# Kernel optimization log

Measured on AMD Instinct MI355X. Metric: run time of the kernel, lower is better.

## Reference

```python
import jax, jax.numpy as jnp
import numpy as np

# dims
B, L, H, W, C = 1, 5, 100, 176, 256   # batch, agents, BEV height, BEV width, channels
HEADS, DHEAD, T = 8, 32, 3            # heads, per-head dim, num agent types
D = HEADS * DHEAD                     # == C here (to_qkv inner dim)
SCALE = DHEAD ** -0.5


def setup_inputs() -> dict:
    key = jax.random.key(0)
    ks = jax.random.split(key, 14)
    x = jax.random.normal(ks[0], (B, L, H, W, C), jnp.float32)
    mask = jnp.ones((B, H, W, 1, L), jnp.int32)
    types = jax.random.randint(ks[1], (B, L), 0, T)
    # prior_encoding: [B, L, 1, 1, 3] = (velocity, dt, type); only type (channel 2) is used
    prior_encoding = jnp.zeros((B, L, 1, 1, 3), jnp.float32).at[..., 2].set(
        types[:, :, None, None].astype(jnp.float32))
    s = C ** -0.5
    Wq = jax.random.normal(ks[2], (T, C, D), jnp.float32) * s
    bq = jax.random.normal(ks[3], (T, D), jnp.float32) * 0.01
    Wk = jax.random.normal(ks[4], (T, C, D), jnp.float32) * s
    bk = jax.random.normal(ks[5], (T, D), jnp.float32) * 0.01
    Wv = jax.random.normal(ks[6], (T, C, D), jnp.float32) * s
    bv = jax.random.normal(ks[7], (T, D), jnp.float32) * 0.01
    Wa = jax.random.normal(ks[8], (T, D, C), jnp.float32) * (D ** -0.5)
    ba = jax.random.normal(ks[9], (T, C), jnp.float32) * 0.01
    rel_att = jax.random.normal(ks[10], (T * T, HEADS, DHEAD, DHEAD), jnp.float32) * (DHEAD ** -0.5)
    rel_msg = jax.random.normal(ks[11], (T * T, HEADS, DHEAD, DHEAD), jnp.float32) * (DHEAD ** -0.5)
    return dict(x=x, mask=mask, prior_encoding=prior_encoding,
                Wq=Wq, bq=bq, Wk=Wk, bk=bk, Wv=Wv, bv=bv, Wa=Wa, ba=ba,
                rel_att=rel_att, rel_msg=rel_msg)


def _split_heads(t):
    # [B,H,W,L,D] -> [B,m,H,W,L,p]
    return jnp.transpose(t.reshape(B, H, W, L, HEADS, DHEAD), (0, 4, 1, 2, 3, 5))


def reference(x, mask, prior_encoding, Wq, bq, Wk, bk, Wv, bv, Wa, ba, rel_att, rel_msg):
    types = prior_encoding[:, :, 0, 0, 2].astype(jnp.int32)      # [B,L]
    xp = jnp.transpose(x, (0, 2, 3, 1, 4))                        # [B,H,W,L,C]

    def proj(Wt, bt):
        # per-agent-type linear: gather weights per agent, then batched matmul
        return jnp.einsum('bhwlc,blcd->bhwld', xp, Wt[types]) + bt[types][:, None, None]

    q = _split_heads(proj(Wq, bq))                                # [B,m,H,W,L,p]
    k = _split_heads(proj(Wk, bk))
    v = _split_heads(proj(Wv, bv))

    etype = types[:, :, None] * T + types[:, None, :]             # [B,L,L]
    w_att = jnp.transpose(rel_att[etype], (0, 3, 1, 2, 4, 5))     # [B,m,L,L,p,q]
    w_msg = jnp.transpose(rel_msg[etype], (0, 3, 1, 2, 4, 5))     # [B,m,L,L,p,c]

    att = jnp.einsum('bmhwip,bmijpq,bmhwjq->bmhwij', q, w_att, k) * SCALE
    att = jnp.where(mask[:, None] == 0, -jnp.inf, att)            # mask [B,1,H,W,1,L]
    att = jax.nn.softmax(att, axis=-1)

    v_msg = jnp.einsum('bmijpc,bmhwjp->bmhwijc', w_msg, v)        # relation-weighted messages
    out = jnp.einsum('bmhwij,bmhwijc->bmhwic', att, v_msg)        # [B,m,H,W,L,c]

    out = jnp.transpose(out, (0, 2, 3, 4, 1, 5)).reshape(B, H, W, L, D)
    out = jnp.einsum('bhwld,bldc->bhwlc', out, Wa[types]) + ba[types][:, None, None]
    return jnp.transpose(out, (0, 3, 1, 2, 4))                    # [B,L,H,W,C]
```

## Files before the change

### kernel.cpp

```cpp
#include <hip/hip_runtime.h>
#include <math.h>

#define HW     17600
#define CD     256
#define LAG    5
#define NHEAD  8
#define DH     32
#define NT     3

typedef short bf16x8 __attribute__((ext_vector_type(8)));
typedef float f32x4  __attribute__((ext_vector_type(4)));

__device__ __forceinline__ float bflo(unsigned u) { return __uint_as_float(u << 16); }
__device__ __forceinline__ float bfhi(unsigned u) { return __uint_as_float(u & 0xffff0000u); }
__device__ __forceinline__ unsigned f2bf(float f) {
    unsigned u = __float_as_uint(f);
    return (u + 0x7fffu + ((u >> 16) & 1u)) >> 16;
}
__device__ __forceinline__ unsigned pack2(float a, float b) {
    return f2bf(a) | (f2bf(b) << 16);
}

__global__ __launch_bounds__(256) void convert_w_kernel(
    const float* __restrict__ Wq, const float* __restrict__ Wk,
    const float* __restrict__ Wv, const float* __restrict__ Wa,
    unsigned short* __restrict__ Wt)
{
    __shared__ float tile[64][65];
    const int mat = blockIdx.y;
    const int k0 = (blockIdx.x >> 2) * 64;
    const int n0 = (blockIdx.x & 3) * 64;
    const float* W;
    if      (mat < 3) W = Wq + (long)mat * 65536;
    else if (mat < 6) W = Wk + (long)(mat - 3) * 65536;
    else if (mat < 9) W = Wv + (long)(mat - 6) * 65536;
    else              W = Wa + (long)(mat - 9) * 65536;
    const int t = threadIdx.x;
#pragma unroll
    for (int r = 0; r < 16; ++r) {
        int idx = r * 256 + t;
        int row = idx >> 6, col = idx & 63;
        tile[row][col] = W[(long)(k0 + row) * 256 + n0 + col];
    }
    __syncthreads();
    unsigned short* dst = Wt + (long)mat * 65536;
#pragma unroll
    for (int r = 0; r < 16; ++r) {
        int idx = r * 256 + t;
        int row = idx >> 6, col = idx & 63;
        dst[(long)(n0 + row) * 256 + k0 + col] = (unsigned short)f2bf(tile[col][row]);
    }
}

__global__ __launch_bounds__(256) void convert_rel_kernel(
    const float* __restrict__ rel_att, const float* __restrict__ rel_msg,
    unsigned short* __restrict__ rattT, unsigned short* __restrict__ rmsgT)
{
    const long base = ((long)(blockIdx.x * NHEAD + blockIdx.y)) << 10;
    const int t = threadIdx.x;
#pragma unroll
    for (int i = 0; i < 4; ++i) {
        int idx = t * 4 + i;
        int p = idx >> 5, q = idx & 31;
        rattT[base + q * 32 + p] = (unsigned short)f2bf(rel_att[base + idx]);
        rmsgT[base + q * 32 + p] = (unsigned short)f2bf(rel_msg[base + idx]);
    }
}

template<bool AF32, bool YBF>
__device__ __forceinline__ void gemm_mfma_core(
    const void* __restrict__ Aptr, long lda,
    const unsigned short* __restrict__ Wt,
    const float* __restrict__ bias,
    void* __restrict__ Yptr, long ldy)
{
    __shared__ unsigned short As[64 * 64];
    __shared__ unsigned short Ws[256 * 64];

    const int t  = threadIdx.x;
    const int m0 = blockIdx.x * 64;
    const int w  = t >> 6;
    const int l  = t & 63;
    const int wr = w >> 1;
    const int wc = w & 1;
    const int fr = l & 15;
    const int ko = (l >> 4) << 3;

    const int srow = t >> 3;
    const int colu = (t & 7) << 3;
    const int scol = colu ^ ((srow & 7) << 3);
    const int axor = (fr & 7) << 3;

    f32x4 acc[2][8];
#pragma unroll
    for (int i = 0; i < 2; ++i)
#pragma unroll
        for (int j = 0; j < 8; ++j) {
            acc[i][j][0] = 0.f; acc[i][j][1] = 0.f;
            acc[i][j][2] = 0.f; acc[i][j][3] = 0.f;
        }

    for (int ks = 0; ks < 4; ++ks) {
        const int k0 = ks << 6;
        __syncthreads();
#pragma unroll
        for (int r = 0; r < 2; ++r) {
            int row = r * 32 + srow;
            if (AF32) {
                const float* src = (const float*)Aptr + (long)(m0 + row) * lda + k0 + colu;
                float4 f0 = *(const float4*)src;
                float4 f1 = *(const float4*)(src + 4);
                uint4 u;
                u.x = pack2(f0.x, f0.y); u.y = pack2(f0.z, f0.w);
                u.z = pack2(f1.x, f1.y); u.w = pack2(f1.z, f1.w);
                *(uint4*)(&As[row * 64 + scol]) = u;
            } else {
                const unsigned short* src =
                    (const unsigned short*)Aptr + (long)(m0 + row) * lda + k0 + colu;
                *(uint4*)(&As[row * 64 + scol]) = *(const uint4*)src;
            }
        }
#pragma unroll
        for (int r = 0; r < 8; ++r) {
            int row = r * 32 + srow;
            *(uint4*)(&Ws[row * 64 + scol]) =
                *(const uint4*)(Wt + (long)row * 256 + k0 + colu);
        }
        __syncthreads();
#pragma unroll
        for (int kk = 0; kk < 2; ++kk) {
            const int fcol = ((kk << 5) | ko) ^ axor;
            bf16x8 a[2], b[8];
#pragma unroll
            for (int i = 0; i < 2; ++i)
                a[i] = *(const bf16x8*)(&As[(wr * 32 + i * 16 + fr) * 64 + fcol]);
#pragma unroll
            for (int j = 0; j < 8; ++j)
                b[j] = *(const bf16x8*)(&Ws[(wc * 128 + j * 16 + fr) * 64 + fcol]);
#pragma unroll
            for (int i = 0; i < 2; ++i)
#pragma unroll
                for (int j = 0; j < 8; ++j)
                    acc[i][j] = __builtin_amdgcn_mfma_f32_16x16x32_bf16(
                        a[i], b[j], acc[i][j], 0, 0, 0);
        }
    }

    const int fq = l >> 4;
#pragma unroll
    for (int j = 0; j < 8; ++j) {
        int col = wc * 128 + j * 16 + fr;
        float bz = bias[col];
#pragma unroll
        for (int i = 0; i < 2; ++i) {
            int rowb = m0 + wr * 32 + i * 16 + (fq << 2);
#pragma unroll
            for (int e = 0; e < 4; ++e) {
                float v = acc[i][j][e] + bz;
                if (YBF)
                    ((unsigned short*)Yptr)[(long)(rowb + e) * ldy + col] =
                        (unsigned short)f2bf(v);
                else
                    ((float*)Yptr)[(long)(rowb + e) * ldy + col] = v;
            }
        }
    }
}

__global__ __launch_bounds__(256) void gemm_qkv_mfma(
    const float* __restrict__ x, const float* __restrict__ pe,
    const unsigned short* __restrict__ Wt,
    const float* __restrict__ bq, const float* __restrict__ bk,
    const float* __restrict__ bv,
    unsigned short* __restrict__ qws, unsigned short* __restrict__ kws,
    unsigned short* __restrict__ vws)
{
    const int lag = blockIdx.z;
    const int tpe = (int)pe[lag * 3 + 2];
    const float* A = x + (long)lag * HW * CD;

#pragma unroll 1
    for (int proj = 0; proj < 3; ++proj) {
        const unsigned short* Wm = Wt + (long)(proj * 3 + tpe) * 65536;
        const float* bias;
        unsigned short* Y;
        long ldy;
        if      (proj == 0) { bias = bq; Y = qws + (long)lag * CD; ldy = LAG * CD; }
        else if (proj == 1) { bias = bk; Y = kws + (long)lag * HW * CD; ldy = CD; }
        else                { bias = bv; Y = vws + (long)lag * HW * CD; ldy = CD; }
        bias += tpe * CD;
        gemm_mfma_core<true, true>(A, CD, Wm, bias, Y, ldy);
        __syncthreads();
    }
}

__global__ __launch_bounds__(256) void gemm_out_mfma(
    const unsigned short* __restrict__ aws, const float* __restrict__ pe,
    const unsigned short* __restrict__ Wt, const float* __restrict__ ba,
    float* __restrict__ out)
{
    const int lag = blockIdx.z;
    const int tpe = (int)pe[lag * 3 + 2];
    const unsigned short* A = aws + (long)lag * CD;
    const unsigned short* Wm = Wt + (long)(9 + tpe) * 65536;
    const float* bias = ba + tpe * CD;
    float* Y = out + (long)lag * HW * CD;
    gemm_mfma_core<false, false>(A, (long)LAG * CD, Wm, bias, Y, CD);
}

#define VGROW 168

__global__ __launch_bounds__(256) void attn_fused_kernel(
    const unsigned short* __restrict__ qws,
    const unsigned short* __restrict__ kws,
    const unsigned short* __restrict__ vws,
    const unsigned short* __restrict__ rattT,
    const unsigned short* __restrict__ rmsgT,
    const int* __restrict__ mask, const float* __restrict__ pe,
    unsigned short* __restrict__ aws)
{
    __shared__ unsigned short lds[4 * 16 * VGROW];

    const int t    = threadIdx.x;
    const int w    = t >> 6;
    const int l    = t & 63;
    const int fr   = l & 15;
    const int fq   = l >> 4;
    const int m    = blockIdx.y;
    const int pix0 = blockIdx.x * 64;

    const int pl2   = t >> 2;
    const int sub   = t & 3;
    const int gpix2 = pix0 + pl2;
    const int wbase = w * 16 * VGROW;
    const int qtb   = wbase + (pl2 & 15) * VGROW;

    int ty[LAG];
#pragma unroll
    for (int i = 0; i < LAG; ++i) ty[i] = (int)pe[i * 3 + 2];
    bool pres[NT] = {false, false, false};
#pragma unroll
    for (int i = 0; i < LAG; ++i) {
        pres[0] = pres[0] || (ty[i] == 0);
        pres[1] = pres[1] || (ty[i] == 1);
        pres[2] = pres[2] || (ty[i] == 2);
    }

    uint4 kf[LAG];
    int mk[LAG];
#pragma unroll
    for (int j = 0; j < LAG; ++j) {
        kf[j] = *(const uint4*)(kws + ((long)j * HW + gpix2) * CD + m * DH + sub * 8);
        mk[j] = mask[gpix2 * LAG + j];
    }
    bf16x8 aq[LAG];
#pragma unroll
    for (int i = 0; i < LAG; ++i)
        aq[i] = *(const bf16x8*)(qws + (long)(pix0 + w * 16 + fr) * (LAG * CD)
                                 + i * CD + m * DH + fq * 8);

    float kx[LAG][8];
#pragma unroll
    for (int j = 0; j < LAG; ++j) {
        kx[j][0] = bflo(kf[j].x); kx[j][1] = bfhi(kf[j].x);
        kx[j][2] = bflo(kf[j].y); kx[j][3] = bfhi(kf[j].y);
        kx[j][4] = bflo(kf[j].z); kx[j][5] = bfhi(kf[j].z);
        kx[j][6] = bflo(kf[j].w); kx[j][7] = bfhi(kf[j].w);
    }

    const float scale = 0.17677669529663687f;
    float att[LAG][LAG];
    for (int sg = 0; sg < NT; ++sg) {
        if (!pres[sg]) continue;
#pragma unroll
        for (int i = 0; i < LAG; ++i) {
            const int e = ty[i] * NT + sg;
            const unsigned short* bb = rattT + ((long)(e * NHEAD + m) << 10);
            bf16x8 b0 = *(const bf16x8*)(bb + fr * 32 + fq * 8);
            bf16x8 b1 = *(const bf16x8*)(bb + (fr + 16) * 32 + fq * 8);
            f32x4 z = {0.f, 0.f, 0.f, 0.f};
            f32x4 d0 = __builtin_amdgcn_mfma_f32_16x16x32_bf16(aq[i], b0, z, 0, 0, 0);
            f32x4 d1 = __builtin_amdgcn_mfma_f32_16x16x32_bf16(aq[i], b1, z, 0, 0, 0);
#pragma unroll
            for (int e4 = 0; e4 < 4; ++e4) {
                const int idx = wbase + (fq * 4 + e4) * VGROW + i * 32;
                lds[idx + fr]      = (unsigned short)f2bf(d0[e4]);
                lds[idx + fr + 16] = (unsigned short)f2bf(d1[e4]);
            }
        }
        __syncthreads();
#pragma unroll
        for (int j = 0; j < LAG; ++j) {
            if (ty[j] != sg) continue;
#pragma unroll
            for (int i = 0; i < LAG; ++i) {
                uint4 qv = *(const uint4*)(&lds[qtb + i * 32 + sub * 8]);
                float part;
                part = bflo(qv.x) * kx[j][0];
                part = fmaf(bfhi(qv.x), kx[j][1], part);
                part = fmaf(bflo(qv.y), kx[j][2], part);
                part = fmaf(bfhi(qv.y), kx[j][3], part);
                part = fmaf(bflo(qv.z), kx[j][4], part);
                part = fmaf(bfhi(qv.z), kx[j][5], part);
                part = fmaf(bflo(qv.w), kx[j][6], part);
                part = fmaf(bfhi(qv.w), kx[j][7], part);
                part += __shfl_xor(part, 1);
                part += __shfl_xor(part, 2);
                att[i][j] = part * scale;
            }
        }
        __syncthreads();
    }

#pragma unroll
    for (int i = 0; i < LAG; ++i) {
        float mx = -INFINITY;
#pragma unroll
        for (int j = 0; j < LAG; ++j) {
            att[i][j] = mk[j] ? att[i][j] : -INFINITY;
            mx = fmaxf(mx, att[i][j]);
        }
        float ssum = 0.f;
#pragma unroll
        for (int j = 0; j < LAG; ++j) {
            att[i][j] = __expf(att[i][j] - mx);
            ssum += att[i][j];
        }
        float inv = 1.f / ssum;
#pragma unroll
        for (int j = 0; j < LAG; ++j) att[i][j] *= inv;
    }

    float vx[LAG][8];
#pragma unroll
    for (int j = 0; j < LAG; ++j) {
        uint4 vf = *(const uint4*)(vws + ((long)j * HW + gpix2) * CD + m * DH + sub * 8);
        vx[j][0] = bflo(vf.x); vx[j][1] = bfhi(vf.x);
        vx[j][2] = bflo(vf.y); vx[j][3] = bfhi(vf.y);
        vx[j][4] = bflo(vf.z); vx[j][5] = bfhi(vf.z);
        vx[j][6] = bflo(vf.w); vx[j][7] = bfhi(vf.w);
    }

    f32x4 oacc[LAG][2];
#pragma unroll
    for (int i = 0; i < LAG; ++i)
#pragma unroll
        for (int c = 0; c < 2; ++c) {
            oacc[i][c][0] = 0.f; oacc[i][c][1] = 0.f;
            oacc[i][c][2] = 0.f; oacc[i][c][3] = 0.f;
        }

    for (int sg = 0; sg < NT; ++sg) {
        if (!pres[sg]) continue;
#pragma unroll
        for (int i = 0; i < LAG; ++i) {
            float vg[8] = {0.f,0.f,0.f,0.f,0.f,0.f,0.f,0.f};
#pragma unroll
            for (int j = 0; j < LAG; ++j) {
                float wj = (ty[j] == sg) ? att[i][j] : 0.f;
#pragma unroll
                for (int d = 0; d < 8; ++d) vg[d] = fmaf(wj, vx[j][d], vg[d]);
            }
            uint4 o;
            o.x = pack2(vg[0], vg[1]); o.y = pack2(vg[2], vg[3]);
            o.z = pack2(vg[4], vg[5]); o.w = pack2(vg[6], vg[7]);
            *(uint4*)(&lds[qtb + i * 32 + sub * 8]) = o;
        }
        __syncthreads();
#pragma unroll
        for (int i = 0; i < LAG; ++i) {
            bf16x8 a = *(const bf16x8*)(&lds[wbase + fr * VGROW + i * 32 + fq * 8]);
            const int e = ty[i] * NT + sg;
            const unsigned short* bb = rmsgT + ((long)(e * NHEAD + m) << 10);
            bf16x8 b0 = *(const bf16x8*)(bb + fr * 32 + fq * 8);
            bf16x8 b1 = *(const bf16x8*)(bb + (fr + 16) * 32 + fq * 8);
            oacc[i][0] = __builtin_amdgcn_mfma_f32_16x16x32_bf16(a, b0, oacc[i][0], 0, 0, 0);
            oacc[i][1] = __builtin_amdgcn_mfma_f32_16x16x32_bf16(a, b1, oacc[i][1], 0, 0, 0);
        }
        __syncthreads();
    }

#pragma unroll
    for (int i = 0; i < LAG; ++i) {
#pragma unroll
        for (int e4 = 0; e4 < 4; ++e4) {
            const long ob = (long)(pix0 + w * 16 + fq * 4 + e4) * (LAG * CD)
                            + i * CD + m * DH;
            aws[ob + fr]      = (unsigned short)f2bf(oacc[i][0][e4]);
            aws[ob + fr + 16] = (unsigned short)f2bf(oacc[i][1][e4]);
        }
    }
}

extern "C" void kernel_launch(void* const* d_in, const int* in_sizes, int n_in,
                              void* d_out, int out_size, void* d_ws, size_t ws_size,
                              hipStream_t stream) {
    const float* x    = (const float*)d_in[0];
    const int*   mask = (const int*)  d_in[1];
    const float* pe   = (const float*)d_in[2];
    const float* Wq   = (const float*)d_in[3];
    const float* bq   = (const float*)d_in[4];
    const float* Wk   = (const float*)d_in[5];
    const float* bk   = (const float*)d_in[6];
    const float* Wv   = (const float*)d_in[7];
    const float* bv   = (const float*)d_in[8];
    const float* Wa   = (const float*)d_in[9];
    const float* ba   = (const float*)d_in[10];
    const float* ratt = (const float*)d_in[11];
    const float* rmsg = (const float*)d_in[12];
    float* out = (float*)d_out;

    const size_t PLANE = (size_t)LAG * HW * CD;

    unsigned short* qws   = (unsigned short*)d_ws;
    unsigned short* kws   = qws + PLANE;
    unsigned short* vws   = kws + PLANE;
    unsigned short* aws   = vws + PLANE;
    unsigned short* Wt    = aws + PLANE;
    unsigned short* rattT = Wt + 786432;
    unsigned short* rmsgT = rattT + 73728;

    convert_w_kernel<<<dim3(16, 12), 256, 0, stream>>>(Wq, Wk, Wv, Wa, Wt);
    convert_rel_kernel<<<dim3(9, 8), 256, 0, stream>>>(ratt, rmsg, rattT, rmsgT);

    gemm_qkv_mfma<<<dim3(HW / 64, 1, LAG), 256, 0, stream>>>(
        x, pe, Wt, bq, bk, bv, qws, kws, vws);

    attn_fused_kernel<<<dim3(HW / 64, NHEAD), 256, 0, stream>>>(
        qws, kws, vws, rattT, rmsgT, mask, pe, aws);

    gemm_out_mfma<<<dim3(HW / 64, 1, LAG), 256, 0, stream>>>(aws, pe, Wt, ba, out);
}
```

Before: 212.6 us.

## Replace block barriers with wave-local LDS fences and prefetch V early

```diff
diff --git a/kernel.cpp b/kernel.cpp
--- a/kernel.cpp
+++ b/kernel.cpp
@@ -210,6 +210,11 @@
 
 #define VGROW 168
 
+__device__ __forceinline__ void wave_lds_fence() {
+    asm volatile("s_waitcnt lgkmcnt(0)" ::: "memory");
+    __builtin_amdgcn_sched_barrier(0);
+}
+
 __global__ __launch_bounds__(256) void attn_fused_kernel(
     const unsigned short* __restrict__ qws,
     const unsigned short* __restrict__ kws,
@@ -246,11 +251,13 @@
         pres[2] = pres[2] || (ty[i] == 2);
     }
 
-    uint4 kf[LAG];
+    uint4 kf[LAG], vf[LAG];
     int mk[LAG];
 #pragma unroll
     for (int j = 0; j < LAG; ++j) {
-        kf[j] = *(const uint4*)(kws + ((long)j * HW + gpix2) * CD + m * DH + sub * 8);
+        const long off = ((long)j * HW + gpix2) * CD + m * DH + sub * 8;
+        kf[j] = *(const uint4*)(kws + off);
+        vf[j] = *(const uint4*)(vws + off);
         mk[j] = mask[gpix2 * LAG + j];
     }
     bf16x8 aq[LAG];
@@ -270,6 +277,7 @@
 
     const float scale = 0.17677669529663687f;
     float att[LAG][LAG];
+#pragma unroll 1
     for (int sg = 0; sg < NT; ++sg) {
         if (!pres[sg]) continue;
 #pragma unroll
@@ -288,28 +296,33 @@
                 lds[idx + fr + 16] = (unsigned short)f2bf(d1[e4]);
             }
         }
-        __syncthreads();
-#pragma unroll
-        for (int j = 0; j < LAG; ++j) {
-            if (ty[j] != sg) continue;
-#pragma unroll
-            for (int i = 0; i < LAG; ++i) {
-                uint4 qv = *(const uint4*)(&lds[qtb + i * 32 + sub * 8]);
+        wave_lds_fence();
+#pragma unroll
+        for (int i = 0; i < LAG; ++i) {
+            uint4 qv = *(const uint4*)(&lds[qtb + i * 32 + sub * 8]);
+            float qx[8];
+            qx[0] = bflo(qv.x); qx[1] = bfhi(qv.x);
+            qx[2] = bflo(qv.y); qx[3] = bfhi(qv.y);
+            qx[4] = bflo(qv.z); qx[5] = bfhi(qv.z);
+            qx[6] = bflo(qv.w); qx[7] = bfhi(qv.w);
+#pragma unroll
+            for (int j = 0; j < LAG; ++j) {
+                if (ty[j] != sg) continue;
                 float part;
-                part = bflo(qv.x) * kx[j][0];
-                part = fmaf(bfhi(qv.x), kx[j][1], part);
-                part = fmaf(bflo(qv.y), kx[j][2], part);
-                part = fmaf(bfhi(qv.y), kx[j][3], part);
-                part = fmaf(bflo(qv.z), kx[j][4], part);
-                part = fmaf(bfhi(qv.z), kx[j][5], part);
-                part = fmaf(bflo(qv.w), kx[j][6], part);
-                part = fmaf(bfhi(qv.w), kx[j][7], part);
+                part = qx[0] * kx[j][0];
+                part = fmaf(qx[1], kx[j][1], part);
+                part = fmaf(qx[2], kx[j][2], part);
+                part = fmaf(qx[3], kx[j][3], part);
+                part = fmaf(qx[4], kx[j][4], part);
+                part = fmaf(qx[5], kx[j][5], part);
+                part = fmaf(qx[6], kx[j][6], part);
+                part = fmaf(qx[7], kx[j][7], part);
                 part += __shfl_xor(part, 1);
                 part += __shfl_xor(part, 2);
                 att[i][j] = part * scale;
             }
         }
-        __syncthreads();
+        asm volatile("" ::: "memory");
     }
 
 #pragma unroll
@@ -334,11 +347,10 @@
     float vx[LAG][8];
 #pragma unroll
     for (int j = 0; j < LAG; ++j) {
-        uint4 vf = *(const uint4*)(vws + ((long)j * HW + gpix2) * CD + m * DH + sub * 8);
-        vx[j][0] = bflo(vf.x); vx[j][1] = bfhi(vf.x);
-        vx[j][2] = bflo(vf.y); vx[j][3] = bfhi(vf.y);
-        vx[j][4] = bflo(vf.z); vx[j][5] = bfhi(vf.z);
-        vx[j][6] = bflo(vf.w); vx[j][7] = bfhi(vf.w);
+        vx[j][0] = bflo(vf[j].x); vx[j][1] = bfhi(vf[j].x);
+        vx[j][2] = bflo(vf[j].y); vx[j][3] = bfhi(vf[j].y);
+        vx[j][4] = bflo(vf[j].z); vx[j][5] = bfhi(vf[j].z);
+        vx[j][6] = bflo(vf[j].w); vx[j][7] = bfhi(vf[j].w);
     }
 
     f32x4 oacc[LAG][2];
@@ -350,6 +362,7 @@
             oacc[i][c][2] = 0.f; oacc[i][c][3] = 0.f;
         }
 
+#pragma unroll 1
     for (int sg = 0; sg < NT; ++sg) {
         if (!pres[sg]) continue;
 #pragma unroll
@@ -357,7 +370,8 @@
             float vg[8] = {0.f,0.f,0.f,0.f,0.f,0.f,0.f,0.f};
 #pragma unroll
             for (int j = 0; j < LAG; ++j) {
-                float wj = (ty[j] == sg) ? att[i][j] : 0.f;
+                if (ty[j] != sg) continue;
+                float wj = att[i][j];
 #pragma unroll
                 for (int d = 0; d < 8; ++d) vg[d] = fmaf(wj, vx[j][d], vg[d]);
             }
@@ -366,7 +380,7 @@
             o.z = pack2(vg[4], vg[5]); o.w = pack2(vg[6], vg[7]);
             *(uint4*)(&lds[qtb + i * 32 + sub * 8]) = o;
         }
-        __syncthreads();
+        wave_lds_fence();
 #pragma unroll
         for (int i = 0; i < LAG; ++i) {
             bf16x8 a = *(const bf16x8*)(&lds[wbase + fr * VGROW + i * 32 + fq * 8]);
@@ -377,7 +391,7 @@
             oacc[i][0] = __builtin_amdgcn_mfma_f32_16x16x32_bf16(a, b0, oacc[i][0], 0, 0, 0);
             oacc[i][1] = __builtin_amdgcn_mfma_f32_16x16x32_bf16(a, b1, oacc[i][1], 0, 0, 0);
         }
-        __syncthreads();
+        asm volatile("" ::: "memory");
     }
 
 #pragma unroll
```

Result: slower. 292.5 us (+37.6%).
